# Optimization experiments

Hardware: AMD Instinct MI355X
Metric: run time of the kernel (lower is better)

Reference implementation:

```python
import jax, jax.numpy as jnp
import numpy as np

DIM = 64
LEN = 256


def setup_inputs() -> dict:
    key = jax.random.key(0)
    ks = jax.random.split(key, 9)
    b, h, B = 4, 8, 16
    q = jax.random.normal(ks[0], (b, h, B, LEN, DIM), dtype=jnp.float32)
    k = jax.random.normal(ks[1], (b, h, B, LEN, DIM), dtype=jnp.float32)
    s = 1.0 / np.sqrt(DIM)
    Wq = jax.random.normal(ks[2], (1, DIM), dtype=jnp.float32) * s
    bq = jnp.ones((1,), dtype=jnp.float32)
    Wk = jax.random.normal(ks[3], (1, DIM), dtype=jnp.float32) * s
    bk = jnp.ones((1,), dtype=jnp.float32)
    sl = 1.0 / np.sqrt(LEN)
    W1 = jax.random.normal(ks[4], (1, LEN), dtype=jnp.float32) * sl
    W2a = jax.random.normal(ks[5], (LEN, LEN), dtype=jnp.float32) * sl
    W2b = jax.random.normal(ks[6], (1, LEN), dtype=jnp.float32) * sl
    return {"q": q, "k": k, "Wq": Wq, "bq": bq, "Wk": Wk, "bk": bk,
            "W1": W1, "W2a": W2a, "W2b": W2b}


def reference(q, k, Wq, bq, Wk, bk, W1, W2a, W2b):
    # Sigma_q/k: [b,h,B,L,1]
    Sigma_q = jnp.einsum('bhgid,od->bhgio', q, Wq) + bq
    Sigma_k = jnp.einsum('bhgjd,od->bhgjo', k, Wk) + bk
    # similarity: [b,h,B,L,L]
    sim = jnp.einsum('bhgid,bhgjd->bhgij', q, k)
    # outer product of the scalar projections: [b,h,B,L,L]
    Sigma = Sigma_q * jnp.swapaxes(Sigma_k, -1, -2)
    # zero the diagonal (sim - diag_embed(diag(sim)))
    eye = jnp.eye(sim.shape[-1], dtype=sim.dtype)
    sim_norm = sim * (1.0 - eye)
    # mlp1: Linear(L,1) over last axis -> [b,h,B,L]
    theta = jnp.einsum('bhgij,j->bhgi', sim_norm, W1[0])
    # mlp2: Linear(L,L) -> LeakyReLU(0.1) -> Linear(L,1) over axis i -> [b,h,B,1]
    hdn = jnp.einsum('bhgi,oi->bhgo', theta, W2a)
    hdn = jnp.where(hdn >= 0, hdn, 0.1 * hdn)
    theta = jnp.einsum('bhgi,oi->bhgo', hdn, W2b)[..., None]  # [b,h,B,1,1]
    sim = sim * Sigma
    attn = jax.nn.softmax(sim, axis=-1) * (sim > theta)
    return attn
```

## Files before the change

### kernel.cpp

```cpp
#include <hip/hip_runtime.h>
#include <math.h>

#define LL 256
#define DD 64

typedef __attribute__((ext_vector_type(8))) short bf16x8;
typedef __attribute__((ext_vector_type(4))) float f32x4;

static __device__ __forceinline__ unsigned short f2bf(float f) {
    union { float f; unsigned u; } v; v.f = f;
    unsigned r = v.u + 0x7fffu + ((v.u >> 16) & 1u);
    return (unsigned short)(r >> 16);
}
static __device__ __forceinline__ float bf2f(unsigned short h) {
    union { unsigned u; float f; } v; v.u = ((unsigned)h) << 16;
    return v.f;
}

__launch_bounds__(512, 2)
__global__ void fused_attn_mfma(const float* __restrict__ q,
                                const float* __restrict__ k,
                                const float* __restrict__ Wq,
                                const float* __restrict__ bq,
                                const float* __restrict__ Wk,
                                const float* __restrict__ bk,
                                const float* __restrict__ W1,
                                const float* __restrict__ W2a,
                                const float* __restrict__ W2b,
                                float* __restrict__ out)
{
    extern __shared__ char smc[];
    unsigned short* kHi = (unsigned short*)smc;
    unsigned short* kLo = (unsigned short*)(smc + 32768);
    float* sPq  = (float*)(smc + 65536);
    float* sPk  = sPq + 256;
    float* sPqk = sPk + 256;
    float* sTh  = sPqk + 256;
    float* sSq  = sTh + 256;
    float* sSk  = sSq + 256;
    float* kwred= sSk + 256;
    float* kw_s = kwred + 512;
    float* sRed = kw_s + 64;

    const int tid  = threadIdx.x;
    const int lane = tid & 63;
    const int wid  = tid >> 6;
    const int r16  = lane & 15;
    const int g4   = lane >> 4;
    const int rbase = wid * 32;
    const int gidx = blockIdx.x;
    const size_t gbase = (size_t)gidx * (LL * DD);
    const float* qg = q + gbase;
    const float4* q4 = (const float4*)qg;
    const float4* k4 = (const float4*)(k + gbase);

    float4 aq[2][2][2];
#pragma unroll
    for (int tr = 0; tr < 2; ++tr)
#pragma unroll
        for (int kk = 0; kk < 2; ++kk) {
            const float* p = qg + (rbase + tr * 16 + r16) * DD + kk * 32 + g4 * 8;
            aq[tr][kk][0] = ((const float4*)p)[0];
            aq[tr][kk][1] = ((const float4*)p)[1];
        }

    const int dc = tid & 15;
    const float4 wq4 = ((const float4*)Wq)[dc];
    const float4 wk4 = ((const float4*)Wk)[dc];
    float kw0 = 0.f, kw1 = 0.f, kw2 = 0.f, kw3 = 0.f;

#pragma unroll
    for (int it = 0; it < 8; ++it) {
        const int f = it * 512 + tid;
        const int j = f >> 4;
        const float4 vq = q4[f];
        const float4 vk = k4[f];

        const int sw = (j & 7) << 4;
        const int boff = j * 128 + ((dc * 8) ^ sw);
        const unsigned short h0 = f2bf(vk.x), h1 = f2bf(vk.y),
                             h2 = f2bf(vk.z), h3 = f2bf(vk.w);
        uint2 hv, lv;
        hv.x = (unsigned)h0 | ((unsigned)h1 << 16);
        hv.y = (unsigned)h2 | ((unsigned)h3 << 16);
        const unsigned short l0 = f2bf(vk.x - bf2f(h0)), l1 = f2bf(vk.y - bf2f(h1)),
                             l2 = f2bf(vk.z - bf2f(h2)), l3 = f2bf(vk.w - bf2f(h3));
        lv.x = (unsigned)l0 | ((unsigned)l1 << 16);
        lv.y = (unsigned)l2 | ((unsigned)l3 << 16);
        *(uint2*)((char*)kHi + boff) = hv;
        *(uint2*)((char*)kLo + boff) = lv;

        const float w1j = W1[j];
        kw0 += w1j * vk.x; kw1 += w1j * vk.y; kw2 += w1j * vk.z; kw3 += w1j * vk.w;

        float pq  = vq.x * wq4.x + vq.y * wq4.y + vq.z * wq4.z + vq.w * wq4.w;
        float pk  = vk.x * wk4.x + vk.y * wk4.y + vk.z * wk4.z + vk.w * wk4.w;
        float pqk = vq.x * vk.x + vq.y * vk.y + vq.z * vk.z + vq.w * vk.w;
#pragma unroll
        for (int m = 1; m < 16; m <<= 1) {
            pq  += __shfl_xor(pq,  m);
            pk  += __shfl_xor(pk,  m);
            pqk += __shfl_xor(pqk, m);
        }
        if (dc == 0) { sPq[j] = pq; sPk[j] = pk; sPqk[j] = pqk; }
    }
    kw0 += __shfl_xor(kw0, 16); kw0 += __shfl_xor(kw0, 32);
    kw1 += __shfl_xor(kw1, 16); kw1 += __shfl_xor(kw1, 32);
    kw2 += __shfl_xor(kw2, 16); kw2 += __shfl_xor(kw2, 32);
    kw3 += __shfl_xor(kw3, 16); kw3 += __shfl_xor(kw3, 32);
    if (lane < 16) {
        float4 kv; kv.x = kw0; kv.y = kw1; kv.z = kw2; kv.w = kw3;
        ((float4*)kwred)[wid * 16 + lane] = kv;
    }

    bf16x8 qhi[2][2], qlo[2][2];
#pragma unroll
    for (int tr = 0; tr < 2; ++tr)
#pragma unroll
        for (int kk = 0; kk < 2; ++kk) {
            const float fv[8] = {aq[tr][kk][0].x, aq[tr][kk][0].y, aq[tr][kk][0].z, aq[tr][kk][0].w,
                                 aq[tr][kk][1].x, aq[tr][kk][1].y, aq[tr][kk][1].z, aq[tr][kk][1].w};
#pragma unroll
            for (int e = 0; e < 8; ++e) {
                const unsigned short h = f2bf(fv[e]);
                qhi[tr][kk][e] = (short)h;
                qlo[tr][kk][e] = (short)f2bf(fv[e] - bf2f(h));
            }
        }

    __syncthreads();
    if (tid < 64) {
        float s = 0.f;
#pragma unroll
        for (int w = 0; w < 8; ++w) s += kwred[w * 64 + tid];
        kw_s[tid] = s;
    }
    __syncthreads();

    const float bq0 = bq[0], bk0 = bk[0];
#pragma unroll
    for (int tr = 0; tr < 2; ++tr) {
        const int row = rbase + tr * 16 + r16;
        float s = 0.f;
#pragma unroll
        for (int kk = 0; kk < 2; ++kk) {
            const int d0 = kk * 32 + g4 * 8;
#pragma unroll
            for (int e = 0; e < 8; ++e) {
                const float qf = bf2f((unsigned short)qhi[tr][kk][e]) +
                                 bf2f((unsigned short)qlo[tr][kk][e]);
                s += qf * kw_s[d0 + e];
            }
        }
        s += __shfl_xor(s, 16);
        s += __shfl_xor(s, 32);
        if (g4 == 0) {
            sTh[row] = s - W1[row] * sPqk[row];
            sSq[row] = sPq[row] + bq0;
            sSk[row] = sPk[row] + bk0;
        }
    }
    __syncthreads();

    {
        const int o = tid >> 1, ih = tid & 1;
        const float4* wrow = (const float4*)W2a + o * 64 + ih * 32;
        const float4* th4  = (const float4*)sTh + ih * 32;
        float h = 0.f;
#pragma unroll 8
        for (int c = 0; c < 32; ++c) {
            const float4 wv = wrow[c];
            const float4 tv = th4[c];
            h += wv.x * tv.x + wv.y * tv.y + wv.z * tv.z + wv.w * tv.w;
        }
        h += __shfl_xor(h, 1);
        float contrib = 0.f;
        if (ih == 0) {
            const float hl = (h >= 0.f) ? h : 0.1f * h;
            contrib = hl * W2b[o];
        }
#pragma unroll
        for (int m = 1; m < 64; m <<= 1) contrib += __shfl_xor(contrib, m);
        if (lane == 0) sRed[wid] = contrib;
    }
    __syncthreads();

    f32x4 acc[2][16];
#pragma unroll
    for (int tr = 0; tr < 2; ++tr)
#pragma unroll
        for (int ct = 0; ct < 16; ++ct)
            acc[tr][ct] = (f32x4){0.f, 0.f, 0.f, 0.f};

#pragma unroll
    for (int ct = 0; ct < 16; ++ct) {
        const int rowk = ct * 16 + r16;
        const int sw = (rowk & 7) << 4;
        const char* ph = (const char*)kHi + rowk * 128;
        const char* pl = (const char*)kLo + rowk * 128;
        const bf16x8 bh0 = *(const bf16x8*)(ph + ((g4 * 16) ^ sw));
        const bf16x8 bh1 = *(const bf16x8*)(ph + ((64 + g4 * 16) ^ sw));
        const bf16x8 bl0 = *(const bf16x8*)(pl + ((g4 * 16) ^ sw));
        const bf16x8 bl1 = *(const bf16x8*)(pl + ((64 + g4 * 16) ^ sw));
#pragma unroll
        for (int tr = 0; tr < 2; ++tr) {
            f32x4 c = acc[tr][ct];
            c = __builtin_amdgcn_mfma_f32_16x16x32_bf16(qhi[tr][0], bh0, c, 0, 0, 0);
            c = __builtin_amdgcn_mfma_f32_16x16x32_bf16(qhi[tr][1], bh1, c, 0, 0, 0);
            c = __builtin_amdgcn_mfma_f32_16x16x32_bf16(qhi[tr][0], bl0, c, 0, 0, 0);
            c = __builtin_amdgcn_mfma_f32_16x16x32_bf16(qhi[tr][1], bl1, c, 0, 0, 0);
            c = __builtin_amdgcn_mfma_f32_16x16x32_bf16(qlo[tr][0], bh0, c, 0, 0, 0);
            c = __builtin_amdgcn_mfma_f32_16x16x32_bf16(qlo[tr][1], bh1, c, 0, 0, 0);
            c = __builtin_amdgcn_mfma_f32_16x16x32_bf16(qlo[tr][0], bl0, c, 0, 0, 0);
            c = __builtin_amdgcn_mfma_f32_16x16x32_bf16(qlo[tr][1], bl1, c, 0, 0, 0);
            acc[tr][ct] = c;
        }
    }

    const float th_sc = sRed[0] + sRed[1] + sRed[2] + sRed[3] +
                        sRed[4] + sRed[5] + sRed[6] + sRed[7];
    float skv[16];
#pragma unroll
    for (int ct = 0; ct < 16; ++ct) skv[ct] = sSk[ct * 16 + r16];

    float* og = out + (size_t)gidx * (LL * LL);
#pragma unroll
    for (int tr = 0; tr < 2; ++tr) {
#pragma unroll
        for (int r = 0; r < 4; ++r) {
            const int row = rbase + tr * 16 + g4 * 4 + r;
            const float sq = sSq[row];
            float lg[16];
            float mx = -INFINITY;
#pragma unroll
            for (int ct = 0; ct < 16; ++ct) {
                lg[ct] = acc[tr][ct][r] * sq * skv[ct];
                mx = fmaxf(mx, lg[ct]);
            }
            mx = fmaxf(mx, __shfl_xor(mx, 1));
            mx = fmaxf(mx, __shfl_xor(mx, 2));
            mx = fmaxf(mx, __shfl_xor(mx, 4));
            mx = fmaxf(mx, __shfl_xor(mx, 8));
            float sum = 0.f;
#pragma unroll
            for (int ct = 0; ct < 16; ++ct) {
                const float pe = __expf(lg[ct] - mx);
                sum += pe;
                lg[ct] = (lg[ct] > th_sc) ? pe : 0.f;
            }
            sum += __shfl_xor(sum, 1);
            sum += __shfl_xor(sum, 2);
            sum += __shfl_xor(sum, 4);
            sum += __shfl_xor(sum, 8);
            const float rinv = 1.0f / sum;
#pragma unroll
            for (int ct = 0; ct < 16; ++ct)
                og[row * LL + ct * 16 + r16] = lg[ct] * rinv;
        }
    }
}

extern "C" void kernel_launch(void* const* d_in, const int* in_sizes, int n_in,
                              void* d_out, int out_size, void* d_ws, size_t ws_size,
                              hipStream_t stream) {
    const float* q   = (const float*)d_in[0];
    const float* k   = (const float*)d_in[1];
    const float* Wq  = (const float*)d_in[2];
    const float* bq  = (const float*)d_in[3];
    const float* Wk  = (const float*)d_in[4];
    const float* bk  = (const float*)d_in[5];
    const float* W1  = (const float*)d_in[6];
    const float* W2a = (const float*)d_in[7];
    const float* W2b = (const float*)d_in[8];
    float* out = (float*)d_out;

    const int ngroup = in_sizes[0] / (LL * DD);
    const size_t lds_bytes = 65536 + 2120 * sizeof(float);

    (void)hipFuncSetAttribute((const void*)fused_attn_mfma,
                              hipFuncAttributeMaxDynamicSharedMemorySize,
                              (int)lds_bytes);

    fused_attn_mfma<<<dim3(ngroup), dim3(512), lds_bytes, stream>>>(
        q, k, Wq, bq, Wk, bk, W1, W2a, W2b, out);
}
```

Baseline: 227.0 us.

## Interleave MFMA chunks with threshold MLP, drop lo*lo term, raise occupancy

Splits the sim MFMA loop into three chunks placed between the theta/MLP phases so matrix work overlaps the scalar reductions and barrier waits. Drops the qlo*klo MFMA terms, cutting MFMA count from 8 to 6 per tile, with a small precision loss. Replaces the 16-lane shuffle reductions for the Sigma projections and q·k diagonal with a per-thread 2-lane row reduction, and vectorizes the kw_s reads. Raises launch_bounds min blocks to 4, which may force register spills given 128 accumulator floats per thread.

```diff
diff --git a/kernel.cpp b/kernel.cpp
--- a/kernel.cpp
+++ b/kernel.cpp
@@ -17,7 +17,7 @@
     return v.f;
 }
 
-__launch_bounds__(512, 2)
+__launch_bounds__(512, 4)
 __global__ void fused_attn_mfma(const float* __restrict__ q,
                                 const float* __restrict__ k,
                                 const float* __restrict__ Wq,
@@ -65,17 +65,12 @@
         }
 
     const int dc = tid & 15;
-    const float4 wq4 = ((const float4*)Wq)[dc];
-    const float4 wk4 = ((const float4*)Wk)[dc];
     float kw0 = 0.f, kw1 = 0.f, kw2 = 0.f, kw3 = 0.f;
-
 #pragma unroll
     for (int it = 0; it < 8; ++it) {
         const int f = it * 512 + tid;
         const int j = f >> 4;
-        const float4 vq = q4[f];
         const float4 vk = k4[f];
-
         const int sw = (j & 7) << 4;
         const int boff = j * 128 + ((dc * 8) ^ sw);
         const unsigned short h0 = f2bf(vk.x), h1 = f2bf(vk.y),
@@ -92,18 +87,28 @@
 
         const float w1j = W1[j];
         kw0 += w1j * vk.x; kw1 += w1j * vk.y; kw2 += w1j * vk.z; kw3 += w1j * vk.w;
-
-        float pq  = vq.x * wq4.x + vq.y * wq4.y + vq.z * wq4.z + vq.w * wq4.w;
-        float pk  = vk.x * wk4.x + vk.y * wk4.y + vk.z * wk4.z + vk.w * wk4.w;
-        float pqk = vq.x * vk.x + vq.y * vk.y + vq.z * vk.z + vq.w * vk.w;
-#pragma unroll
-        for (int m = 1; m < 16; m <<= 1) {
-            pq  += __shfl_xor(pq,  m);
-            pk  += __shfl_xor(pk,  m);
-            pqk += __shfl_xor(pqk, m);
-        }
-        if (dc == 0) { sPq[j] = pq; sPk[j] = pk; sPqk[j] = pqk; }
-    }
+    }
+
+    {
+        const int j2 = tid >> 1, h2 = tid & 1;
+        float pq = 0.f, pk = 0.f, pqk = 0.f;
+#pragma unroll
+        for (int it = 0; it < 8; ++it) {
+            const int idx = j2 * 16 + h2 * 8 + it;
+            const float4 vq = q4[idx];
+            const float4 vk = k4[idx];
+            const float4 wq4 = ((const float4*)Wq)[h2 * 8 + it];
+            const float4 wk4 = ((const float4*)Wk)[h2 * 8 + it];
+            pq  += vq.x * wq4.x + vq.y * wq4.y + vq.z * wq4.z + vq.w * wq4.w;
+            pk  += vk.x * wk4.x + vk.y * wk4.y + vk.z * wk4.z + vk.w * wk4.w;
+            pqk += vq.x * vk.x + vq.y * vk.y + vq.z * vk.z + vq.w * vk.w;
+        }
+        pq  += __shfl_xor(pq,  1);
+        pk  += __shfl_xor(pk,  1);
+        pqk += __shfl_xor(pqk, 1);
+        if (h2 == 0) { sPq[j2] = pq; sPk[j2] = pk; sPqk[j2] = pqk; }
+    }
+
     kw0 += __shfl_xor(kw0, 16); kw0 += __shfl_xor(kw0, 32);
     kw1 += __shfl_xor(kw1, 16); kw1 += __shfl_xor(kw1, 32);
     kw2 += __shfl_xor(kw2, 16); kw2 += __shfl_xor(kw2, 32);
@@ -129,37 +134,77 @@
         }
 
     __syncthreads();
+
     if (tid < 64) {
         float s = 0.f;
 #pragma unroll
         for (int w = 0; w < 8; ++w) s += kwred[w * 64 + tid];
         kw_s[tid] = s;
     }
+
+    f32x4 acc[2][16];
+#pragma unroll
+    for (int tr = 0; tr < 2; ++tr)
+#pragma unroll
+        for (int ct = 0; ct < 16; ++ct)
+            acc[tr][ct] = (f32x4){0.f, 0.f, 0.f, 0.f};
+
+#define MFMA_CHUNK(CT0, CT1)                                                  \
+    _Pragma("unroll")                                                         \
+    for (int ct = (CT0); ct < (CT1); ++ct) {                                  \
+        const int rowk = ct * 16 + r16;                                       \
+        const int sw = (rowk & 7) << 4;                                       \
+        const char* ph = (const char*)kHi + rowk * 128;                       \
+        const char* pl = (const char*)kLo + rowk * 128;                       \
+        const bf16x8 bh0 = *(const bf16x8*)(ph + ((g4 * 16) ^ sw));           \
+        const bf16x8 bh1 = *(const bf16x8*)(ph + ((64 + g4 * 16) ^ sw));      \
+        const bf16x8 bl0 = *(const bf16x8*)(pl + ((g4 * 16) ^ sw));           \
+        const bf16x8 bl1 = *(const bf16x8*)(pl + ((64 + g4 * 16) ^ sw));      \
+        _Pragma("unroll")                                                     \
+        for (int tr = 0; tr < 2; ++tr) {                                      \
+            f32x4 c = acc[tr][ct];                                            \
+            c = __builtin_amdgcn_mfma_f32_16x16x32_bf16(qhi[tr][0], bh0, c, 0, 0, 0); \
+            c = __builtin_amdgcn_mfma_f32_16x16x32_bf16(qhi[tr][1], bh1, c, 0, 0, 0); \
+            c = __builtin_amdgcn_mfma_f32_16x16x32_bf16(qhi[tr][0], bl0, c, 0, 0, 0); \
+            c = __builtin_amdgcn_mfma_f32_16x16x32_bf16(qhi[tr][1], bl1, c, 0, 0, 0); \
+            c = __builtin_amdgcn_mfma_f32_16x16x32_bf16(qlo[tr][0], bh0, c, 0, 0, 0); \
+            c = __builtin_amdgcn_mfma_f32_16x16x32_bf16(qlo[tr][1], bh1, c, 0, 0, 0); \
+            acc[tr][ct] = c;                                                  \
+        }                                                                     \
+    }
+
+    MFMA_CHUNK(0, 6)
     __syncthreads();
 
-    const float bq0 = bq[0], bk0 = bk[0];
-#pragma unroll
-    for (int tr = 0; tr < 2; ++tr) {
-        const int row = rbase + tr * 16 + r16;
-        float s = 0.f;
-#pragma unroll
-        for (int kk = 0; kk < 2; ++kk) {
-            const int d0 = kk * 32 + g4 * 8;
-#pragma unroll
-            for (int e = 0; e < 8; ++e) {
-                const float qf = bf2f((unsigned short)qhi[tr][kk][e]) +
-                                 bf2f((unsigned short)qlo[tr][kk][e]);
-                s += qf * kw_s[d0 + e];
-            }
-        }
-        s += __shfl_xor(s, 16);
-        s += __shfl_xor(s, 32);
-        if (g4 == 0) {
-            sTh[row] = s - W1[row] * sPqk[row];
-            sSq[row] = sPq[row] + bq0;
-            sSk[row] = sPk[row] + bk0;
-        }
-    }
+    {
+        const float bq0 = bq[0], bk0 = bk[0];
+#pragma unroll
+        for (int tr = 0; tr < 2; ++tr) {
+            const int row = rbase + tr * 16 + r16;
+            float s = 0.f;
+#pragma unroll
+            for (int kk = 0; kk < 2; ++kk) {
+                const float4 kwa = *(const float4*)(kw_s + kk * 32 + g4 * 8);
+                const float4 kwb = *(const float4*)(kw_s + kk * 32 + g4 * 8 + 4);
+                const float kwv[8] = {kwa.x, kwa.y, kwa.z, kwa.w, kwb.x, kwb.y, kwb.z, kwb.w};
+#pragma unroll
+                for (int e = 0; e < 8; ++e) {
+                    const float qf = bf2f((unsigned short)qhi[tr][kk][e]) +
+                                     bf2f((unsigned short)qlo[tr][kk][e]);
+                    s += qf * kwv[e];
+                }
+            }
+            s += __shfl_xor(s, 16);
+            s += __shfl_xor(s, 32);
+            if (g4 == 0) {
+                sTh[row] = s - W1[row] * sPqk[row];
+                sSq[row] = sPq[row] + bq0;
+                sSk[row] = sPk[row] + bk0;
+            }
+        }
+    }
+
+    MFMA_CHUNK(6, 12)
     __syncthreads();
 
     {
@@ -183,39 +228,9 @@
         for (int m = 1; m < 64; m <<= 1) contrib += __shfl_xor(contrib, m);
         if (lane == 0) sRed[wid] = contrib;
     }
+
+    MFMA_CHUNK(12, 16)
     __syncthreads();
-
-    f32x4 acc[2][16];
-#pragma unroll
-    for (int tr = 0; tr < 2; ++tr)
-#pragma unroll
-        for (int ct = 0; ct < 16; ++ct)
-            acc[tr][ct] = (f32x4){0.f, 0.f, 0.f, 0.f};
-
-#pragma unroll
-    for (int ct = 0; ct < 16; ++ct) {
-        const int rowk = ct * 16 + r16;
-        const int sw = (rowk & 7) << 4;
-        const char* ph = (const char*)kHi + rowk * 128;
-        const char* pl = (const char*)kLo + rowk * 128;
-        const bf16x8 bh0 = *(const bf16x8*)(ph + ((g4 * 16) ^ sw));
-        const bf16x8 bh1 = *(const bf16x8*)(ph + ((64 + g4 * 16) ^ sw));
-        const bf16x8 bl0 = *(const bf16x8*)(pl + ((g4 * 16) ^ sw));
-        const bf16x8 bl1 = *(const bf16x8*)(pl + ((64 + g4 * 16) ^ sw));
-#pragma unroll
-        for (int tr = 0; tr < 2; ++tr) {
-            f32x4 c = acc[tr][ct];
-            c = __builtin_amdgcn_mfma_f32_16x16x32_bf16(qhi[tr][0], bh0, c, 0, 0, 0);
-            c = __builtin_amdgcn_mfma_f32_16x16x32_bf16(qhi[tr][1], bh1, c, 0, 0, 0);
-            c = __builtin_amdgcn_mfma_f32_16x16x32_bf16(qhi[tr][0], bl0, c, 0, 0, 0);
-            c = __builtin_amdgcn_mfma_f32_16x16x32_bf16(qhi[tr][1], bl1, c, 0, 0, 0);
-            c = __builtin_amdgcn_mfma_f32_16x16x32_bf16(qlo[tr][0], bh0, c, 0, 0, 0);
-            c = __builtin_amdgcn_mfma_f32_16x16x32_bf16(qlo[tr][1], bh1, c, 0, 0, 0);
-            c = __builtin_amdgcn_mfma_f32_16x16x32_bf16(qlo[tr][0], bl0, c, 0, 0, 0);
-            c = __builtin_amdgcn_mfma_f32_16x16x32_bf16(qlo[tr][1], bl1, c, 0, 0, 0);
-            acc[tr][ct] = c;
-        }
-    }
 
     const float th_sc = sRed[0] + sRed[1] + sRed[2] + sRed[3] +
                         sRed[4] + sRed[5] + sRed[6] + sRed[7];
```

After: 271.8 us. +19.8%, slower.
